# Kernel optimization log

Measured on AMD Instinct MI355X. Metric: run time of the kernel, lower is better.

Reference implementation:

```python
import jax, jax.numpy as jnp
import numpy as np
from jax import lax

OUT_SCALE = 0.001


def setup_inputs() -> dict:
    key = jax.random.key(0)
    kz, kx = jax.random.split(key)
    z = jax.random.normal(kz, (64, 256, 7, 7), dtype=jnp.float32)
    x = jax.random.normal(kx, (64, 256, 31, 31), dtype=jnp.float32)
    return {"z": z, "x": x}


def reference(z, x):
    # depthwise cross-correlation: each (batch, channel) slice of z is slid
    # over the matching slice of x. Implemented as a grouped conv with
    # feature_group_count = B*C, exactly mirroring torch F.conv2d(groups=B*C).
    B, C, kh, kw = z.shape
    H, W = x.shape[2], x.shape[3]
    x_r = x.reshape(1, B * C, H, W)           # [1, B*C, H, W]
    k_r = z.reshape(B * C, 1, kh, kw)          # [B*C, 1, kh, kw] (OIHW)
    out = lax.conv_general_dilated(
        x_r, k_r,
        window_strides=(1, 1),
        padding="VALID",
        feature_group_count=B * C,
        dimension_numbers=("NCHW", "OIHW", "NCHW"),
    )  # [1, B*C, H-kh+1, W-kw+1]
    out = out.reshape(B, C, out.shape[2], out.shape[3])
    return out * OUT_SCALE
```

## Files before the change

### kernel.cpp

```cpp
#include <hip/hip_runtime.h>


#define KH 7
#define KW 7
#define XH 31
#define XW 31
#define OH 25
#define OW 25
#define NSLICE (64 * 256)
#define THREADS 128
#define SPW 2
#define SPB (SPW * 2)
#define XSW_DW 2048
#define SLICE_X (XH * XW)
#define SLICE_O (OH * OW)
#define X_TOTAL_DW (NSLICE * SLICE_X)

__device__ __forceinline__ void gl_lds16(const float* g, float* l) {
    __builtin_amdgcn_global_load_lds(
        (const __attribute__((address_space(1))) void*)g,
        (__attribute__((address_space(3))) void*)l, 16, 0, 0);
}

__global__ __launch_bounds__(THREADS, 4)
void xcorr_dw_kernel(const float* __restrict__ z,
                     const float* __restrict__ x,
                     float* __restrict__ out) {
    __shared__ float xs[2][XSW_DW];
    const int tid  = threadIdx.x;
    const int lane = tid & 63;
    const int wv   = __builtin_amdgcn_readfirstlane(tid >> 6);
    float* __restrict__ xsw = xs[wv];

    const int wslice = blockIdx.x * SPB + wv * SPW;
    const int g0r = wslice * SLICE_X;
    const int pre = g0r & 3;
    const int g0  = g0r - pre;

    #pragma unroll
    for (int k = 0; k < 8; ++k) {
        const int dw  = k * 256 + lane * 4;
        const int gdw = min(g0 + dw, X_TOTAL_DW - 4);
        gl_lds16(x + gdw, xsw + dw);
    }

    const float* __restrict__ zw = z + (size_t)wslice * (KH * KW);
    float* __restrict__ og = out + (size_t)wslice * SLICE_O;

    const int h   = (lane >= OH) ? 1 : 0;
    const int oy  = h ? (lane - OH) : lane;
    const bool act = (lane < 2 * OH);
    const int c0  = h ? 13 : 0;

    asm volatile("s_waitcnt vmcnt(4)" ::: "memory");
    __builtin_amdgcn_sched_barrier(0);
    if (act) {
        float acc[13] = {};
        const float* __restrict__ xrow = xsw + pre;
        #pragma unroll
        for (int i = 0; i < KH; ++i) {
            const float* __restrict__ p = xrow + (oy + i) * XW + c0;
            float f[19];
            #pragma unroll
            for (int c = 0; c < 19; ++c) f[c] = p[c];
            #pragma unroll
            for (int j = 0; j < KW; ++j) {
                const float w = zw[i * KW + j];
                #pragma unroll
                for (int c = 0; c < 13; ++c)
                    acc[c] = fmaf(f[c + j], w, acc[c]);
            }
        }
        const int fb = oy * OW + c0;
        #pragma unroll
        for (int c = 0; c < 12; ++c) xsw[fb + c] = acc[c] * 0.001f;
        if (!h) xsw[fb + 12] = acc[12] * 0.001f;
    }

    asm volatile("s_waitcnt vmcnt(0)" ::: "memory");
    __builtin_amdgcn_sched_barrier(0);
    #pragma unroll
    for (int k = 0; k < 9; ++k) og[k * 64 + lane] = xsw[k * 64 + lane];
    if (lane < SLICE_O - 576) og[576 + lane] = xsw[576 + lane];

    if (act) {
        float acc[13] = {};
        const float* __restrict__ xrow = xsw + pre + SLICE_X;
        const float* __restrict__ zs = zw + KH * KW;
        #pragma unroll
        for (int i = 0; i < KH; ++i) {
            const float* __restrict__ p = xrow + (oy + i) * XW + c0;
            float f[19];
            #pragma unroll
            for (int c = 0; c < 19; ++c) f[c] = p[c];
            #pragma unroll
            for (int j = 0; j < KW; ++j) {
                const float w = zs[i * KW + j];
                #pragma unroll
                for (int c = 0; c < 13; ++c)
                    acc[c] = fmaf(f[c + j], w, acc[c]);
            }
        }
        const int fb = SLICE_O + oy * OW + c0;
        #pragma unroll
        for (int c = 0; c < 12; ++c) xsw[fb + c] = acc[c] * 0.001f;
        if (!h) xsw[fb + 12] = acc[12] * 0.001f;
    }
    #pragma unroll
    for (int k = 0; k < 9; ++k)
        og[SLICE_O + k * 64 + lane] = xsw[SLICE_O + k * 64 + lane];
    if (lane < SLICE_O - 576)
        og[SLICE_O + 576 + lane] = xsw[SLICE_O + 576 + lane];
}

extern "C" void kernel_launch(void* const* d_in, const int* in_sizes, int n_in,
                              void* d_out, int out_size, void* d_ws, size_t ws_size,
                              hipStream_t stream) {
    const float* z = (const float*)d_in[0];
    const float* x = (const float*)d_in[1];
    float* out = (float*)d_out;
    const int nblk = NSLICE / SPB;
    xcorr_dw_kernel<<<dim3(nblk), dim3(THREADS), 0, stream>>>(z, x, out);
}
```

Before: 113.8 us.

## Make kernel persistent with double-buffered LDS prefetch of slice pairs

Replaces the one-block-per-four-slices grid with a fixed grid of 1280 blocks whose waves loop over slice pairs. Each wave keeps two LDS buffers and prefetches the next pair via global_load_lds while computing the current one. The aim is to overlap global loads with compute and cut launch/tail overhead. It doubles LDS per block, which may lower occupancy, and it relies on manual vmcnt/lgkmcnt waits that could race if the counts are wrong.

Result: slower. 125.2 us (+10.0%).

```diff
diff --git a/kernel.cpp b/kernel.cpp
--- a/kernel.cpp
+++ b/kernel.cpp
@@ -9,9 +9,10 @@
 #define OW 25
 #define NSLICE (64 * 256)
 #define THREADS 128
-#define SPW 2
-#define SPB (SPW * 2)
-#define XSW_DW 2048
+#define NPAIR (NSLICE / 2)
+#define NBLK 1280
+#define NWAVE (NBLK * 2)
+#define BUF_DW 2048
 #define SLICE_X (XH * XW)
 #define SLICE_O (OH * OW)
 #define X_TOTAL_DW (NSLICE * SLICE_X)
@@ -22,41 +23,29 @@
         (__attribute__((address_space(3))) void*)l, 16, 0, 0);
 }
 
-__global__ __launch_bounds__(THREADS, 4)
-void xcorr_dw_kernel(const float* __restrict__ z,
-                     const float* __restrict__ x,
-                     float* __restrict__ out) {
-    __shared__ float xs[2][XSW_DW];
-    const int tid  = threadIdx.x;
-    const int lane = tid & 63;
-    const int wv   = __builtin_amdgcn_readfirstlane(tid >> 6);
-    float* __restrict__ xsw = xs[wv];
-
-    const int wslice = blockIdx.x * SPB + wv * SPW;
-    const int g0r = wslice * SLICE_X;
-    const int pre = g0r & 3;
-    const int g0  = g0r - pre;
-
+__device__ __forceinline__ void stage_pair(const float* __restrict__ x,
+                                           float* __restrict__ buf,
+                                           int pair, int lane) {
+    const int g0r = pair * (2 * SLICE_X);
+    const int g0  = g0r - (g0r & 3);
     #pragma unroll
     for (int k = 0; k < 8; ++k) {
         const int dw  = k * 256 + lane * 4;
         const int gdw = min(g0 + dw, X_TOTAL_DW - 4);
-        gl_lds16(x + gdw, xsw + dw);
+        gl_lds16(x + gdw, buf + dw);
     }
+}
 
-    const float* __restrict__ zw = z + (size_t)wslice * (KH * KW);
-    float* __restrict__ og = out + (size_t)wslice * SLICE_O;
-
-    const int h   = (lane >= OH) ? 1 : 0;
-    const int oy  = h ? (lane - OH) : lane;
-    const bool act = (lane < 2 * OH);
-    const int c0  = h ? 13 : 0;
-
-    asm volatile("s_waitcnt vmcnt(4)" ::: "memory");
-    __builtin_amdgcn_sched_barrier(0);
+__device__ __forceinline__ void compute_slice(float* __restrict__ buf,
+                                              const float* __restrict__ zsl,
+                                              int pre, int s,
+                                              int oy, int c0, bool act) {
+    float wz[KH * KW];
+    #pragma unroll
+    for (int t = 0; t < KH * KW; ++t) wz[t] = zsl[t];
     if (act) {
         float acc[13] = {};
-        const float* __restrict__ xrow = xsw + pre;
+        const float* __restrict__ xrow = buf + pre + s * SLICE_X;
         #pragma unroll
         for (int i = 0; i < KH; ++i) {
             const float* __restrict__ p = xrow + (oy + i) * XW + c0;
@@ -65,52 +54,63 @@
             for (int c = 0; c < 19; ++c) f[c] = p[c];
             #pragma unroll
             for (int j = 0; j < KW; ++j) {
-                const float w = zw[i * KW + j];
+                const float w = wz[i * KW + j];
                 #pragma unroll
                 for (int c = 0; c < 13; ++c)
                     acc[c] = fmaf(f[c + j], w, acc[c]);
             }
         }
-        const int fb = oy * OW + c0;
+        const int fb = s * SLICE_O + oy * OW + c0;
         #pragma unroll
-        for (int c = 0; c < 12; ++c) xsw[fb + c] = acc[c] * 0.001f;
-        if (!h) xsw[fb + 12] = acc[12] * 0.001f;
+        for (int c = 0; c < 12; ++c) buf[fb + c] = acc[c] * 0.001f;
+        if (c0 == 0) buf[fb + 12] = acc[12] * 0.001f;
     }
+}
 
-    asm volatile("s_waitcnt vmcnt(0)" ::: "memory");
-    __builtin_amdgcn_sched_barrier(0);
-    #pragma unroll
-    for (int k = 0; k < 9; ++k) og[k * 64 + lane] = xsw[k * 64 + lane];
-    if (lane < SLICE_O - 576) og[576 + lane] = xsw[576 + lane];
+__global__ __launch_bounds__(THREADS, 4)
+void xcorr_dw_kernel(const float* __restrict__ z,
+                     const float* __restrict__ x,
+                     float* __restrict__ out) {
+    __shared__ float xs[2][2][BUF_DW];
+    const int tid  = threadIdx.x;
+    const int lane = tid & 63;
+    const int wv   = __builtin_amdgcn_readfirstlane(tid >> 6);
+    const int wid  = blockIdx.x * 2 + wv;
 
-    if (act) {
-        float acc[13] = {};
-        const float* __restrict__ xrow = xsw + pre + SLICE_X;
-        const float* __restrict__ zs = zw + KH * KW;
+    const int h   = (lane >= OH) ? 1 : 0;
+    const int oy  = h ? (lane - OH) : lane;
+    const int c0  = h ? 13 : 0;
+    const bool act = (lane < 2 * OH);
+
+    float* b0 = xs[wv][0];
+    float* b1 = xs[wv][1];
+
+    stage_pair(x, b0, wid, lane);
+    if (wid + NWAVE < NPAIR) stage_pair(x, b1, wid + NWAVE, lane);
+
+    #pragma unroll 1
+    for (int p = wid; p < NPAIR; p += NWAVE) {
+        asm volatile("s_waitcnt vmcnt(8)" ::: "memory");
+        __builtin_amdgcn_sched_barrier(0);
+
+        const int wslice = 2 * p;
+        const int pre    = (2 * p) & 3;
+        const float* __restrict__ zp = z + (size_t)wslice * (KH * KW);
+
+        compute_slice(b0, zp,           pre, 0, oy, c0, act);
+        compute_slice(b0, zp + KH * KW, pre, 1, oy, c0, act);
+
+        float* __restrict__ og = out + (size_t)wslice * SLICE_O;
         #pragma unroll
-        for (int i = 0; i < KH; ++i) {
-            const float* __restrict__ p = xrow + (oy + i) * XW + c0;
-            float f[19];
-            #pragma unroll
-            for (int c = 0; c < 19; ++c) f[c] = p[c];
-            #pragma unroll
-            for (int j = 0; j < KW; ++j) {
-                const float w = zs[i * KW + j];
-                #pragma unroll
-                for (int c = 0; c < 13; ++c)
-                    acc[c] = fmaf(f[c + j], w, acc[c]);
-            }
-        }
-        const int fb = SLICE_O + oy * OW + c0;
-        #pragma unroll
-        for (int c = 0; c < 12; ++c) xsw[fb + c] = acc[c] * 0.001f;
-        if (!h) xsw[fb + 12] = acc[12] * 0.001f;
+        for (int k = 0; k < 19; ++k) og[k * 64 + lane] = b0[k * 64 + lane];
+        if (lane < 2 * SLICE_O - 19 * 64) og[19 * 64 + lane] = b0[19 * 64 + lane];
+
+        asm volatile("s_waitcnt lgkmcnt(0)" ::: "memory");
+        __builtin_amdgcn_sched_barrier(0);
+        if (p + 2 * NWAVE < NPAIR) stage_pair(x, b0, p + 2 * NWAVE, lane);
+
+        float* t = b0; b0 = b1; b1 = t;
     }
-    #pragma unroll
-    for (int k = 0; k < 9; ++k)
-        og[SLICE_O + k * 64 + lane] = xsw[SLICE_O + k * 64 + lane];
-    if (lane < SLICE_O - 576)
-        og[SLICE_O + 576 + lane] = xsw[SLICE_O + 576 + lane];
 }
 
 extern "C" void kernel_launch(void* const* d_in, const int* in_sizes, int n_in,
@@ -119,6 +119,5 @@
     const float* z = (const float*)d_in[0];
     const float* x = (const float*)d_in[1];
     float* out = (float*)d_out;
-    const int nblk = NSLICE / SPB;
-    xcorr_dw_kernel<<<dim3(nblk), dim3(THREADS), 0, stream>>>(z, x, out);
+    xcorr_dw_kernel<<<dim3(NBLK), dim3(THREADS), 0, stream>>>(z, x, out);
 }
```
